# Optimization experiments

Measured on AMD Instinct MI355X. Metric: run time of the kernel, lower is better.

## Reference

```python
import jax, jax.numpy as jnp
import numpy as np

NUM_ATOMS = 100
D = 32        # initial_atom_dim
H = 16        # hidden_dim (multiplicity per irrep)
NB = 16       # edge_dim / number of bessel basis functions
CUT = 6.0     # radius_cutoff
DEG = 4.0     # degree_norm
OUT = 1       # output_dim
INV4PI = 1.0 / np.sqrt(4.0 * np.pi)  # 'integral' SH normalization


def _bessel(d, nb, cut):
    # e3nn soft_one_hot_linspace(basis='bessel', cutoff=True) * sqrt(nb)
    x = d[:, None]
    n = jnp.arange(1, nb + 1, dtype=d.dtype)
    safe = jnp.maximum(x, 1e-9)
    out = np.sqrt(2.0 / cut) * jnp.sin(n * jnp.pi * x / cut) / safe
    return out * (x < cut) * np.sqrt(float(nb))


def _fc(x, w1, w2):
    # e3nn FullyConnectedNet: fan-in normalized linear layers, silu, no bias
    h = jax.nn.silu(x @ w1 / np.sqrt(x.shape[-1]))
    return h @ w2 / np.sqrt(w1.shape[-1])


def _forward(atomic_numbers, edge_index, coords, atom_emb,
             fc0_w1, fc0_w2, fc1_w1, fc1_w2, w_readout):
    src, dst = edge_index[0], edge_index[1]
    N = coords.shape[0]
    E = src.shape[0]

    vec = coords[src] - coords[dst]                      # [E,3]
    dist = jnp.linalg.norm(vec, axis=-1)                 # [E]
    unit = vec / jnp.maximum(dist, 1e-9)[:, None]

    # spherical harmonics, l=0 and l=1, 'integral' normalization
    y0 = jnp.full((E,), INV4PI, dtype=coords.dtype)      # [E]
    y1 = (np.sqrt(3.0) * INV4PI) * unit                  # [E,3]
    basis = _bessel(dist, NB, CUT)                       # [E,NB]

    x = atom_emb[atomic_numbers]                         # [N,D] (row 0 is padding)

    # ---- layer 0: scalars (D x0e) x (1x0e+1x1o) -> H x0e + H x1o ----
    w = _fc(basis, fc0_w1, fc0_w2)                       # [E, 2*D*H] per-edge TP weights
    wa = w[:, : D * H].reshape(E, D, H)
    wb = w[:, D * H:].reshape(E, D, H)
    xs = x[src]
    n0 = 1.0 / np.sqrt(D)                                # path fan-in norm
    m0 = jnp.einsum('ed,edh->eh', xs, wa) * y0[:, None] * n0          # [E,H]
    m1 = jnp.einsum('ed,edh->eh', xs, wb)[:, :, None] * y1[:, None, :] * n0  # [E,H,3]
    z0 = jax.ops.segment_sum(m0, dst, num_segments=N) / DEG           # [N,H]
    z1 = jax.ops.segment_sum(m1, dst, num_segments=N) / DEG           # [N,H,3]

    # ---- layer 1: (H x0e + H x1o) x (1x0e+1x1o) -> same irreps, skip-connected ----
    w = _fc(basis, fc1_w1, fc1_w2)                       # [E, 4*H*H]
    w1_ = w[:, 0 * H * H:1 * H * H].reshape(E, H, H)     # 0e x 0e -> 0e
    w2_ = w[:, 1 * H * H:2 * H * H].reshape(E, H, H)     # 0e x 1o -> 1o
    w3_ = w[:, 2 * H * H:3 * H * H].reshape(E, H, H)     # 1o x 0e -> 1o
    w4_ = w[:, 3 * H * H:4 * H * H].reshape(E, H, H)     # 1o x 1o -> 0e (CG = dot/sqrt(3))
    s, v = z0[src], z1[src]
    n1 = 1.0 / np.sqrt(2 * H)                            # two paths per output irrep
    dot = jnp.einsum('ehm,em->eh', v, y1) / np.sqrt(3.0)
    o0 = (jnp.einsum('eh,ehk->ek', s, w1_) * y0[:, None]
          + jnp.einsum('eh,ehk->ek', dot, w4_)) * n1
    o1 = (jnp.einsum('eh,ehk->ek', s, w2_)[:, :, None] * y1[:, None, :]
          + jnp.einsum('ehm,ehk->ekm', v, w3_) * y0[:, None, None]) * n1
    z0 = jax.ops.segment_sum(o0, dst, num_segments=N) / DEG + z0      # skip
    z1 = jax.ops.segment_sum(o1, dst, num_segments=N) / DEG + z1

    # ---- scalar readout (o3.Linear onto 0e) + graph sum-pool ----
    node_scalar = z0 @ w_readout / np.sqrt(H)            # [N,OUT]
    return jnp.sum(node_scalar, axis=0)                  # [OUT]


def setup_inputs() -> dict:
    key = jax.random.key(0)
    ks = jax.random.split(key, 9)
    N, E = 10000, 160000
    atomic_numbers = jax.random.randint(ks[0], (N,), 0, NUM_ATOMS)
    coords = jax.random.normal(ks[1], (N, 3), dtype=jnp.float32)
    edge_index = jax.random.randint(ks[2], (2, E), 0, N)
    atom_emb = jax.random.normal(ks[3], (NUM_ATOMS, D), dtype=jnp.float32).at[0].set(0.0)
    fc0_w1 = jax.random.normal(ks[4], (NB, H), dtype=jnp.float32)
    fc0_w2 = jax.random.normal(ks[5], (H, 2 * D * H), dtype=jnp.float32)
    fc1_w1 = jax.random.normal(ks[6], (NB, H), dtype=jnp.float32)
    fc1_w2 = jax.random.normal(ks[7], (H, 4 * H * H), dtype=jnp.float32)
    w_readout = jax.random.normal(ks[8], (H, OUT), dtype=jnp.float32)
    return {"atomic_numbers": atomic_numbers, "coords": coords, "edge_index": edge_index,
            "atom_emb": atom_emb, "fc0_w1": fc0_w1, "fc0_w2": fc0_w2,
            "fc1_w1": fc1_w1, "fc1_w2": fc1_w2, "w_readout": w_readout}


def reference(atomic_numbers, coords, edge_index, atom_emb,
              fc0_w1, fc0_w2, fc1_w1, fc1_w2, w_readout):
    return _forward(atomic_numbers, edge_index, coords, atom_emb,
                    fc0_w1, fc0_w2, fc1_w1, fc1_w2, w_readout)
```

## Files before the change

kernel.cpp:

```cpp
#include <hip/hip_runtime.h>
#include <math.h>


namespace {
constexpr int   NATOMS   = 100;
constexpr float PI_F     = 3.14159265358979323846f;
constexpr float INV4PI_F = 0.28209479177387814f;
constexpr float SQRT3_F  = 1.7320508075688772f;
constexpr float CUT_F    = 6.0f;
constexpr float BASIS_C  = 2.3094010767585034f;
constexpr float N0_F     = 0.17677669529663687f;
constexpr float K0_F = INV4PI_F * N0_F * 0.0625f;
constexpr float K1_F = SQRT3_F * INV4PI_F * N0_F * 0.0625f;
constexpr float P2SC = INV4PI_F * N0_F * (1.0f / 64.0f);
}

__device__ __forceinline__ float silu_fast(float x) {
  return x / (1.0f + __expf(-x));
}

__device__ __forceinline__ float block_reduce_sum(float v) {
  #pragma unroll
  for (int o = 32; o > 0; o >>= 1) v += __shfl_down(v, o, 64);
  __shared__ float ls[8];
  int lane = threadIdx.x & 63;
  int w    = threadIdx.x >> 6;
  if (lane == 0) ls[w] = v;
  __syncthreads();
  float s = 0.f;
  if (threadIdx.x == 0) {
    int nw = (blockDim.x + 63) >> 6;
    for (int i = 0; i < nw; ++i) s += ls[i];
  }
  return s;
}

__global__ void __launch_bounds__(256)
table_kernel(const float* __restrict__ atom_emb,
             const float* __restrict__ fc0_w2,
             float* __restrict__ TI,
             float4* __restrict__ zero4,
             float* __restrict__ out,
             int NZ4) {
  int b = blockIdx.x;
  int tt = threadIdx.x;
  if (b < NATOMS) {
    int j = tt >> 4;
    int h = tt & 15;
    float s0 = 0.f, s1 = 0.f;
    #pragma unroll
    for (int d = 0; d < 32; ++d) {
      float x = atom_emb[b * 32 + d];
      s0 = fmaf(x, fc0_w2[j * 1024 + d * 16 + h], s0);
      s1 = fmaf(x, fc0_w2[j * 1024 + 512 + d * 16 + h], s1);
    }
    TI[b * 512 + j * 32 + 2 * h]     = s0;
    TI[b * 512 + j * 32 + 2 * h + 1] = s1;
    if (b == 0 && tt == 0) *out = 0.f;
  } else {
    int idx = (b - NATOMS) * 256 + tt;
    if (idx < NZ4) zero4[idx] = make_float4(0.f, 0.f, 0.f, 0.f);
  }
}

__global__ void __launch_bounds__(256)
edge_kernel(const int* __restrict__ ei,
            const float* __restrict__ coords,
            const int* __restrict__ an,
            const float* __restrict__ TI,
            const float* __restrict__ fc0_w1,
            const float* __restrict__ fc1_w1,
            float* __restrict__ zacc,
            float* __restrict__ sacc,
            int E) {
  int lane = threadIdx.x & 63;
  int g    = threadIdx.x >> 4;
  int t    = threadIdx.x & 15;
  int base = lane & 48;

  float w0c[16], w1c[16];
  #pragma unroll
  for (int k = 0; k < 16; ++k) {
    w0c[k] = fc0_w1[k * 16 + t];
    w1c[k] = fc1_w1[k * 16 + t];
  }

  const float angc = PI_F / CUT_F;
  int eA = blockIdx.x * 32 + g;
  int eB = eA + 16;
  bool vA = eA < E, vB = eB < E;
  int eAc = vA ? eA : 0, eBc = vB ? eB : 0;

  int sA = ei[eAc], dA = ei[E + eAc];
  int sB = ei[eBc], dB = ei[E + eBc];
  float sxA = coords[3 * sA + 0], syA = coords[3 * sA + 1], szA = coords[3 * sA + 2];
  float dxA = coords[3 * dA + 0], dyA = coords[3 * dA + 1], dzA = coords[3 * dA + 2];
  float sxB = coords[3 * sB + 0], syB = coords[3 * sB + 1], szB = coords[3 * sB + 2];
  float dxB = coords[3 * dB + 0], dyB = coords[3 * dB + 1], dzB = coords[3 * dB + 2];
  int aA = an[sA], aB = an[sB];

  float vxA = sxA - dxA, vyA = syA - dyA, vzA = szA - dzA;
  float vxB = sxB - dxB, vyB = syB - dyB, vzB = szB - dzB;
  float distA = sqrtf(vxA * vxA + vyA * vyA + vzA * vzA);
  float distB = sqrtf(vxB * vxB + vyB * vyB + vzB * vzB);
  float ivA = 1.0f / fmaxf(distA, 1e-9f);
  float ivB = 1.0f / fmaxf(distB, 1e-9f);
  float uxA = vxA * ivA, uyA = vyA * ivA, uzA = vzA * ivA;
  float uxB = vxB * ivB, uyB = vyB * ivB, uzB = vzB * ivB;
  float bcA = (distA < CUT_F) ? (BASIS_C * ivA) : 0.0f;
  float bcB = (distB < CUT_F) ? (BASIS_C * ivB) : 0.0f;

  float angA = angc * distA, angB = angc * distB;
  float scA = __sinf(angA), twA = 2.0f * __cosf(angA), spA = 0.f;
  float scB = __sinf(angB), twB = 2.0f * __cosf(angB), spB = 0.f;
  float a0A = 0.f, a1A = 0.f, a0B = 0.f, a1B = 0.f;
  #pragma unroll
  for (int k = 0; k < 16; ++k) {
    a0A = fmaf(scA, w0c[k], a0A);
    a1A = fmaf(scA, w1c[k], a1A);
    a0B = fmaf(scB, w0c[k], a0B);
    a1B = fmaf(scB, w1c[k], a1B);
    float snA = fmaf(twA, scA, -spA); spA = scA; scA = snA;
    float snB = fmaf(twB, scB, -spB); spB = scB; scB = snB;
  }
  float h0A = silu_fast(a0A * bcA * 0.25f);
  float h1A = silu_fast(a1A * bcA * 0.25f);
  float h0B = silu_fast(a0B * bcB * 0.25f);
  float h1B = silu_fast(a1B * bcB * 0.25f);

  if (vA) {
    float* sa = sacc + (size_t)sA * 64 + t;
    unsafeAtomicAdd(sa,      h1A);
    unsafeAtomicAdd(sa + 16, h1A * uxA);
    unsafeAtomicAdd(sa + 32, h1A * uyA);
    unsafeAtomicAdd(sa + 48, h1A * uzA);
  }
  if (vB) {
    float* sb = sacc + (size_t)sB * 64 + t;
    unsafeAtomicAdd(sb,      h1B);
    unsafeAtomicAdd(sb + 16, h1B * uxB);
    unsafeAtomicAdd(sb + 32, h1B * uyB);
    unsafeAtomicAdd(sb + 48, h1B * uzB);
  }

  const float2* tpA = (const float2*)(TI + aA * 512) + t;
  const float2* tpB = (const float2*)(TI + aB * 512) + t;
  float u0A = 0.f, u1A = 0.f, u0B = 0.f, u1B = 0.f;
  #pragma unroll
  for (int j = 0; j < 16; ++j) {
    float hjA = __shfl(h0A, base + j, 64);
    float hjB = __shfl(h0B, base + j, 64);
    float2 TA = tpA[j * 16];
    float2 TB = tpB[j * 16];
    u0A = fmaf(hjA, TA.x, u0A);
    u1A = fmaf(hjA, TA.y, u1A);
    u0B = fmaf(hjB, TB.x, u0B);
    u1B = fmaf(hjB, TB.y, u1B);
  }

  if (vA) {
    float* za = zacc + (size_t)dA * 64 + t;
    float m1 = K1_F * u1A;
    unsafeAtomicAdd(za,      K0_F * u0A);
    unsafeAtomicAdd(za + 16, m1 * uxA);
    unsafeAtomicAdd(za + 32, m1 * uyA);
    unsafeAtomicAdd(za + 48, m1 * uzA);
  }
  if (vB) {
    float* zb = zacc + (size_t)dB * 64 + t;
    float m1 = K1_F * u1B;
    unsafeAtomicAdd(zb,      K0_F * u0B);
    unsafeAtomicAdd(zb + 16, m1 * uxB);
    unsafeAtomicAdd(zb + 32, m1 * uyB);
    unsafeAtomicAdd(zb + 48, m1 * uzB);
  }
}

__global__ void __launch_bounds__(256)
node_kernel(const float* __restrict__ zacc,
            const float* __restrict__ sacc,
            const float* __restrict__ fc1_w2,
            const float* __restrict__ w_readout,
            float* __restrict__ out,
            int N) {
  __shared__ float ggs[512];
  {
    int j = threadIdx.x >> 4;
    int h = threadIdx.x & 15;
    float g1 = 0.f, g4 = 0.f;
    #pragma unroll
    for (int k = 0; k < 16; ++k) {
      float r = w_readout[k];
      g1 = fmaf(fc1_w2[j * 1024 + h * 16 + k], r, g1);
      g4 = fmaf(fc1_w2[j * 1024 + 768 + h * 16 + k], r, g4);
    }
    ggs[h * 16 + j]       = g1;
    ggs[256 + h * 16 + j] = g4;
  }
  __syncthreads();

  int lane = threadIdx.x & 63;
  int t    = lane & 15;
  int base = lane & 48;
  int node = blockIdx.x * 16 + (threadIdx.x >> 4);
  bool valid = node < N;
  size_t nb = (size_t)(valid ? node : 0) * 64;

  float z0 = zacc[nb + t];
  float zx = zacc[nb + 16 + t];
  float zy = zacc[nb + 32 + t];
  float zz = zacc[nb + 48 + t];
  float A  = sacc[nb + t];
  float Bx = sacc[nb + 16 + t];
  float By = sacc[nb + 32 + t];
  float Bz = sacc[nb + 48 + t];

  float Q = 0.f, Px = 0.f, Py = 0.f, Pz = 0.f;
  #pragma unroll
  for (int h = 0; h < 16; ++h) {
    float z0h = __shfl(z0, base + h, 64);
    float zxh = __shfl(zx, base + h, 64);
    float zyh = __shfl(zy, base + h, 64);
    float zzh = __shfl(zz, base + h, 64);
    float g1 = ggs[h * 16 + t];
    float g4 = ggs[256 + h * 16 + t];
    Q  = fmaf(g1, z0h, Q);
    Px = fmaf(g4, zxh, Px);
    Py = fmaf(g4, zyh, Py);
    Pz = fmaf(g4, zzh, Pz);
  }

  float c = 0.f;
  if (valid) {
    float dotp = fmaf(Q, A, fmaf(Px, Bx, fmaf(Py, By, Pz * Bz)));
    c = fmaf(0.25f * z0, w_readout[t], P2SC * dotp);
  }

  float tot = block_reduce_sum(c);
  if (threadIdx.x == 0) atomicAdd(out, tot);
}

extern "C" void kernel_launch(void* const* d_in, const int* in_sizes, int n_in,
                              void* d_out, int out_size, void* d_ws, size_t ws_size,
                              hipStream_t stream) {
  const int*   an        = (const int*)d_in[0];
  const float* coords    = (const float*)d_in[1];
  const int*   ei        = (const int*)d_in[2];
  const float* atom_emb  = (const float*)d_in[3];
  const float* fc0_w1    = (const float*)d_in[4];
  const float* fc0_w2    = (const float*)d_in[5];
  const float* fc1_w1    = (const float*)d_in[6];
  const float* fc1_w2    = (const float*)d_in[7];
  const float* w_readout = (const float*)d_in[8];

  int N = in_sizes[0];
  int E = in_sizes[2] / 2;

  float* zacc = (float*)d_ws;
  float* sacc = zacc + (size_t)N * 64;
  float* TI   = sacc + (size_t)N * 64;
  float* out  = (float*)d_out;

  int NZ4 = N * 32;
  int zblocks = (NZ4 + 255) / 256;
  table_kernel<<<NATOMS + zblocks, 256, 0, stream>>>(
      atom_emb, fc0_w2, TI, (float4*)zacc, out, NZ4);

  edge_kernel<<<(E + 31) / 32, 256, 0, stream>>>(
      ei, coords, an, TI, fc0_w1, fc1_w1, zacc, sacc, E);

  node_kernel<<<(N + 15) / 16, 256, 0, stream>>>(
      zacc, sacc, fc1_w2, w_readout, out, N);
}
```

Measured before the change: 151.5 us.

## Replace source-side scatter accumulator with second edge pass gathering node features

Removes the sacc scatter (four atomics per edge-lane into source nodes) and the node kernel. Instead, a second persistent edge kernel recomputes each edge's geometry and layer-1 radial MLP, gathers the layer-0 node features from zacc at the source, and contracts them directly into the scalar output. The skip-connection readout term is folded into the first edge kernel's block reduction. This trades half the scattered atomics and the sacc buffer for recomputing geometry and Bessel features plus random gathers of zacc in a second pass.

```diff
diff --git a/kernel.cpp b/kernel.cpp
--- a/kernel.cpp
+++ b/kernel.cpp
@@ -69,21 +69,19 @@
             const int* __restrict__ an,
             const float* __restrict__ TI,
             const float* __restrict__ fc0_w1,
-            const float* __restrict__ fc1_w1,
+            const float* __restrict__ w_readout,
             float* __restrict__ zacc,
-            float* __restrict__ sacc,
+            float* __restrict__ out,
             int E) {
   int lane = threadIdx.x & 63;
   int g    = threadIdx.x >> 4;
   int t    = threadIdx.x & 15;
   int base = lane & 48;
 
-  float w0c[16], w1c[16];
-  #pragma unroll
-  for (int k = 0; k < 16; ++k) {
-    w0c[k] = fc0_w1[k * 16 + t];
-    w1c[k] = fc1_w1[k * 16 + t];
-  }
+  float w0c[16];
+  #pragma unroll
+  for (int k = 0; k < 16; ++k) w0c[k] = fc0_w1[k * 16 + t];
+  float rr = w_readout[t];
 
   const float angc = PI_F / CUT_F;
   int eA = blockIdx.x * 32 + g;
@@ -113,35 +111,16 @@
   float angA = angc * distA, angB = angc * distB;
   float scA = __sinf(angA), twA = 2.0f * __cosf(angA), spA = 0.f;
   float scB = __sinf(angB), twB = 2.0f * __cosf(angB), spB = 0.f;
-  float a0A = 0.f, a1A = 0.f, a0B = 0.f, a1B = 0.f;
+  float a0A = 0.f, a0B = 0.f;
   #pragma unroll
   for (int k = 0; k < 16; ++k) {
     a0A = fmaf(scA, w0c[k], a0A);
-    a1A = fmaf(scA, w1c[k], a1A);
     a0B = fmaf(scB, w0c[k], a0B);
-    a1B = fmaf(scB, w1c[k], a1B);
     float snA = fmaf(twA, scA, -spA); spA = scA; scA = snA;
     float snB = fmaf(twB, scB, -spB); spB = scB; scB = snB;
   }
   float h0A = silu_fast(a0A * bcA * 0.25f);
-  float h1A = silu_fast(a1A * bcA * 0.25f);
   float h0B = silu_fast(a0B * bcB * 0.25f);
-  float h1B = silu_fast(a1B * bcB * 0.25f);
-
-  if (vA) {
-    float* sa = sacc + (size_t)sA * 64 + t;
-    unsafeAtomicAdd(sa,      h1A);
-    unsafeAtomicAdd(sa + 16, h1A * uxA);
-    unsafeAtomicAdd(sa + 32, h1A * uyA);
-    unsafeAtomicAdd(sa + 48, h1A * uzA);
-  }
-  if (vB) {
-    float* sb = sacc + (size_t)sB * 64 + t;
-    unsafeAtomicAdd(sb,      h1B);
-    unsafeAtomicAdd(sb + 16, h1B * uxB);
-    unsafeAtomicAdd(sb + 32, h1B * uyB);
-    unsafeAtomicAdd(sb + 48, h1B * uzB);
-  }
 
   const float2* tpA = (const float2*)(TI + aA * 512) + t;
   const float2* tpB = (const float2*)(TI + aB * 512) + t;
@@ -158,6 +137,7 @@
     u1B = fmaf(hjB, TB.y, u1B);
   }
 
+  float c = 0.f;
   if (vA) {
     float* za = zacc + (size_t)dA * 64 + t;
     float m1 = K1_F * u1A;
@@ -165,6 +145,7 @@
     unsafeAtomicAdd(za + 16, m1 * uxA);
     unsafeAtomicAdd(za + 32, m1 * uyA);
     unsafeAtomicAdd(za + 48, m1 * uzA);
+    c = fmaf(u0A, rr, c);
   }
   if (vB) {
     float* zb = zacc + (size_t)dB * 64 + t;
@@ -173,16 +154,23 @@
     unsafeAtomicAdd(zb + 16, m1 * uxB);
     unsafeAtomicAdd(zb + 32, m1 * uyB);
     unsafeAtomicAdd(zb + 48, m1 * uzB);
-  }
+    c = fmaf(u0B, rr, c);
+  }
+  c *= 0.25f * K0_F;
+
+  float tot = block_reduce_sum(c);
+  if (threadIdx.x == 0) atomicAdd(out, tot);
 }
 
 __global__ void __launch_bounds__(256)
-node_kernel(const float* __restrict__ zacc,
-            const float* __restrict__ sacc,
-            const float* __restrict__ fc1_w2,
-            const float* __restrict__ w_readout,
-            float* __restrict__ out,
-            int N) {
+edge2_kernel(const int* __restrict__ ei,
+             const float* __restrict__ coords,
+             const float* __restrict__ zacc,
+             const float* __restrict__ fc1_w1,
+             const float* __restrict__ fc1_w2,
+             const float* __restrict__ w_readout,
+             float* __restrict__ out,
+             int E) {
   __shared__ float ggs[512];
   {
     int j = threadIdx.x >> 4;
@@ -202,41 +190,83 @@
   int lane = threadIdx.x & 63;
   int t    = lane & 15;
   int base = lane & 48;
-  int node = blockIdx.x * 16 + (threadIdx.x >> 4);
-  bool valid = node < N;
-  size_t nb = (size_t)(valid ? node : 0) * 64;
-
-  float z0 = zacc[nb + t];
-  float zx = zacc[nb + 16 + t];
-  float zy = zacc[nb + 32 + t];
-  float zz = zacc[nb + 48 + t];
-  float A  = sacc[nb + t];
-  float Bx = sacc[nb + 16 + t];
-  float By = sacc[nb + 32 + t];
-  float Bz = sacc[nb + 48 + t];
-
-  float Q = 0.f, Px = 0.f, Py = 0.f, Pz = 0.f;
-  #pragma unroll
-  for (int h = 0; h < 16; ++h) {
-    float z0h = __shfl(z0, base + h, 64);
-    float zxh = __shfl(zx, base + h, 64);
-    float zyh = __shfl(zy, base + h, 64);
-    float zzh = __shfl(zz, base + h, 64);
-    float g1 = ggs[h * 16 + t];
-    float g4 = ggs[256 + h * 16 + t];
-    Q  = fmaf(g1, z0h, Q);
-    Px = fmaf(g4, zxh, Px);
-    Py = fmaf(g4, zyh, Py);
-    Pz = fmaf(g4, zzh, Pz);
-  }
-
-  float c = 0.f;
-  if (valid) {
-    float dotp = fmaf(Q, A, fmaf(Px, Bx, fmaf(Py, By, Pz * Bz)));
-    c = fmaf(0.25f * z0, w_readout[t], P2SC * dotp);
-  }
-
-  float tot = block_reduce_sum(c);
+
+  float g1r[16], g4r[16], w1c[16];
+  #pragma unroll
+  for (int k = 0; k < 16; ++k) {
+    g1r[k] = ggs[t * 16 + k];
+    g4r[k] = ggs[256 + t * 16 + k];
+    w1c[k] = fc1_w1[k * 16 + t];
+  }
+
+  const float angc = PI_F / CUT_F;
+  int ggid = blockIdx.x * 16 + (threadIdx.x >> 4);
+  int ngroups = gridDim.x * 16;
+
+  float c3 = 0.f;
+  for (int e0 = ggid; e0 < E; e0 += 2 * ngroups) {
+    int eA = e0;
+    int eB = e0 + ngroups;
+    bool vB = eB < E;
+    int eBc = vB ? eB : eA;
+
+    int sA = ei[eA],  dA = ei[E + eA];
+    int sB = ei[eBc], dB = ei[E + eBc];
+    float sxA = coords[3 * sA + 0], syA = coords[3 * sA + 1], szA = coords[3 * sA + 2];
+    float dxA = coords[3 * dA + 0], dyA = coords[3 * dA + 1], dzA = coords[3 * dA + 2];
+    float sxB = coords[3 * sB + 0], syB = coords[3 * sB + 1], szB = coords[3 * sB + 2];
+    float dxB = coords[3 * dB + 0], dyB = coords[3 * dB + 1], dzB = coords[3 * dB + 2];
+
+    size_t qa = (size_t)sA * 64;
+    size_t qb = (size_t)sB * 64;
+    float z0A = zacc[qa + t],      z0B = zacc[qb + t];
+    float zxA = zacc[qa + 16 + t], zxB = zacc[qb + 16 + t];
+    float zyA = zacc[qa + 32 + t], zyB = zacc[qb + 32 + t];
+    float zzA = zacc[qa + 48 + t], zzB = zacc[qb + 48 + t];
+
+    float vxA = sxA - dxA, vyA = syA - dyA, vzA = szA - dzA;
+    float vxB = sxB - dxB, vyB = syB - dyB, vzB = szB - dzB;
+    float distA = sqrtf(vxA * vxA + vyA * vyA + vzA * vzA);
+    float distB = sqrtf(vxB * vxB + vyB * vyB + vzB * vzB);
+    float ivA = 1.0f / fmaxf(distA, 1e-9f);
+    float ivB = 1.0f / fmaxf(distB, 1e-9f);
+    float uxA = vxA * ivA, uyA = vyA * ivA, uzA = vzA * ivA;
+    float uxB = vxB * ivB, uyB = vyB * ivB, uzB = vzB * ivB;
+    float bcA = (distA < CUT_F) ? (BASIS_C * ivA) : 0.0f;
+    float bcB = (distB < CUT_F) ? (BASIS_C * ivB) : 0.0f;
+
+    float angA = angc * distA, angB = angc * distB;
+    float scA = __sinf(angA), twA = 2.0f * __cosf(angA), spA = 0.f;
+    float scB = __sinf(angB), twB = 2.0f * __cosf(angB), spB = 0.f;
+    float a1A = 0.f, a1B = 0.f;
+    #pragma unroll
+    for (int k = 0; k < 16; ++k) {
+      a1A = fmaf(scA, w1c[k], a1A);
+      a1B = fmaf(scB, w1c[k], a1B);
+      float snA = fmaf(twA, scA, -spA); spA = scA; scA = snA;
+      float snB = fmaf(twB, scB, -spB); spB = scB; scB = snB;
+    }
+    float h1A = silu_fast(a1A * bcA * 0.25f);
+    float h1B = silu_fast(a1B * bcB * 0.25f);
+
+    float H1A = 0.f, H4A = 0.f, H1B = 0.f, H4B = 0.f;
+    #pragma unroll
+    for (int k = 0; k < 16; ++k) {
+      float hbA = __shfl(h1A, base + k, 64);
+      float hbB = __shfl(h1B, base + k, 64);
+      H1A = fmaf(g1r[k], hbA, H1A);
+      H4A = fmaf(g4r[k], hbA, H4A);
+      H1B = fmaf(g1r[k], hbB, H1B);
+      H4B = fmaf(g4r[k], hbB, H4B);
+    }
+
+    float wA = fmaf(uxA, zxA, fmaf(uyA, zyA, uzA * zzA));
+    float wB = fmaf(uxB, zxB, fmaf(uyB, zyB, uzB * zzB));
+    c3 = fmaf(H1A, z0A, fmaf(H4A, wA, c3));
+    if (vB) c3 = fmaf(H1B, z0B, fmaf(H4B, wB, c3));
+  }
+
+  float tot = block_reduce_sum(c3 * P2SC);
   if (threadIdx.x == 0) atomicAdd(out, tot);
 }
 
@@ -257,18 +287,17 @@
   int E = in_sizes[2] / 2;
 
   float* zacc = (float*)d_ws;
-  float* sacc = zacc + (size_t)N * 64;
-  float* TI   = sacc + (size_t)N * 64;
+  float* TI   = zacc + (size_t)N * 64;
   float* out  = (float*)d_out;
 
-  int NZ4 = N * 32;
+  int NZ4 = N * 16;
   int zblocks = (NZ4 + 255) / 256;
   table_kernel<<<NATOMS + zblocks, 256, 0, stream>>>(
       atom_emb, fc0_w2, TI, (float4*)zacc, out, NZ4);
 
   edge_kernel<<<(E + 31) / 32, 256, 0, stream>>>(
-      ei, coords, an, TI, fc0_w1, fc1_w1, zacc, sacc, E);
-
-  node_kernel<<<(N + 15) / 16, 256, 0, stream>>>(
-      zacc, sacc, fc1_w2, w_readout, out, N);
-}
+      ei, coords, an, TI, fc0_w1, w_readout, zacc, out, E);
+
+  edge2_kernel<<<2048, 256, 0, stream>>>(
+      ei, coords, zacc, fc1_w1, fc1_w2, w_readout, out, E);
+}
```

After: 186.6 us. +23.1%, slower.
